# Optimization experiments

Measured on AMD Instinct MI355X. Metric: run time of the kernel, lower is better.

## Reference

```python
import jax, jax.numpy as jnp
import numpy as np

NUM_EXPERTS = 128
INPUT_DIM = 128
HIDDEN_DIM = 512
OUTPUT_DIM = 128
TOKENS_PER_EXPERT = 2048


def make_identity_experts(num_experts, input_dim, output_dim):
    # identical to the torch helper: zeros with ones on the (square) diagonal
    d = min(input_dim, output_dim)
    w = jnp.zeros((num_experts, input_dim, output_dim), dtype=jnp.float32)
    idx = jnp.arange(d)
    return w.at[:, idx, idx].set(1.0)


def setup_inputs() -> dict:
    key = jax.random.key(0)
    k_tok, = jax.random.split(key, 1)
    group_token = jax.random.normal(
        k_tok, (NUM_EXPERTS, TOKENS_PER_EXPERT, INPUT_DIM), dtype=jnp.float32)
    weights1 = make_identity_experts(NUM_EXPERTS, INPUT_DIM, HIDDEN_DIM)
    weights2 = make_identity_experts(NUM_EXPERTS, HIDDEN_DIM, OUTPUT_DIM)
    return {"group_token": group_token, "weights1": weights1, "weights2": weights2}


def reference(group_token, weights1, weights2):
    # grouped GEMM 1: per-expert [T, in] @ [in, hid]
    h = jnp.einsum('etd,edh->eth', group_token, weights1)
    # exact (erf-based) GELU, matching torch.nn.functional.gelu default
    h = jax.nn.gelu(h, approximate=False)
    # grouped GEMM 2: per-expert [T, hid] @ [hid, out]
    out = jnp.einsum('eth,eho->eto', h, weights2)
    return out
```

## Files before the change

kernel.cpp:

```cpp
#include <hip/hip_runtime.h>
#include <hip/hip_bf16.h>
#include <stdint.h>

typedef __attribute__((ext_vector_type(8))) short s8v;
typedef __attribute__((ext_vector_type(4))) short s4v;
typedef __attribute__((ext_vector_type(4))) float f4v;

#define NE   128
#define NT   2048
#define DIN  128
#define DH   512
#define DOUT 128

#define MFMA32(a,b,c) __builtin_amdgcn_mfma_f32_16x16x32_bf16(a,b,c,0,0,0)
#define MFMA16(a,b,c) __builtin_amdgcn_mfma_f32_16x16x16bf16_1k(a,b,c,0,0,0)

#define GLOAD16(g,l) __builtin_amdgcn_global_load_lds( \
    (const __attribute__((address_space(1))) void*)(g), \
    (__attribute__((address_space(3))) void*)(l), 16, 0, 0)

#define WAIT_VM(N) asm volatile("s_waitcnt vmcnt(" #N ")" ::: "memory")
#define BAR() do { asm volatile("" ::: "memory"); \
                   __builtin_amdgcn_s_barrier();  \
                   asm volatile("" ::: "memory"); } while (0)

__device__ __forceinline__ __hip_bfloat162 pk2(float a, float b) {
  float2 t; t.x = a; t.y = b;
  return __float22bfloat162_rn(t);
}

__device__ __forceinline__ s8v pack8(float4 a, float4 b) {
  union { s8v v; __hip_bfloat162 h[4]; } u;
  u.h[0] = pk2(a.x, a.y); u.h[1] = pk2(a.z, a.w);
  u.h[2] = pk2(b.x, b.y); u.h[3] = pk2(b.z, b.w);
  return u.v;
}

__device__ __forceinline__ float gelu_f(float x) {
  float x2 = x * x;
  float p  = __builtin_fmaf(x2, 0.07135481f, 1.5957691f);
  float e  = __expf(-x * p);
  return x * __builtin_amdgcn_rcpf(1.0f + e);
}

#define W1_BLOCKS (NE * 4)
__global__ __launch_bounds__(256) void pack_weights(
    const float* __restrict__ W1, const float* __restrict__ W2,
    ushort* __restrict__ W1F, ushort* __restrict__ W2F) {
  __shared__ __align__(16) float T[32 * 132];
  const int tid = threadIdx.x;

  if ((int)blockIdx.x < W1_BLOCKS) {
    const int e = blockIdx.x >> 2, ks = blockIdx.x & 3;
    const float* We = W1 + (size_t)e * (DIN * DH) + (size_t)(ks * 32) * DH;
    const int r = tid >> 3, c0 = (tid & 7) * 16;
    const int lane = tid & 63, wid = tid >> 6;
    const int q = lane >> 4, l16 = lane & 15;
    for (int hc = 0; hc < 4; ++hc) {
      if (hc) __syncthreads();
      const float* src = We + (size_t)r * DH + hc * 128 + c0;
      float4 v0 = *(const float4*)(src + 0);
      float4 v1 = *(const float4*)(src + 4);
      float4 v2 = *(const float4*)(src + 8);
      float4 v3 = *(const float4*)(src + 12);
      float* t = &T[r * 132 + c0];
      *(float4*)(t + 0) = v0; *(float4*)(t + 4)  = v1;
      *(float4*)(t + 8) = v2; *(float4*)(t + 12) = v3;
      __syncthreads();
#pragma unroll
      for (int i = 0; i < 2; ++i) {
        const int htl = wid + 4 * i;
        const int ht  = hc * 8 + htl;
        float g[8];
#pragma unroll
        for (int j = 0; j < 8; ++j) g[j] = T[(8 * q + j) * 132 + 16 * htl + l16];
        float4 a; a.x = g[0]; a.y = g[1]; a.z = g[2]; a.w = g[3];
        float4 b; b.x = g[4]; b.y = g[5]; b.z = g[6]; b.w = g[7];
        *(s8v*)(W1F + ((((size_t)e * 32 + ht) * 4) + ks) * 512 + lane * 8) = pack8(a, b);
      }
    }
  } else {
    const int bb = (int)blockIdx.x - W1_BLOCKS;
    const int e = bb >> 5, ht = bb & 31;
    float (*T2)[132] = (float (*)[132])T;
    const int h = tid >> 4, c16 = tid & 15;
    const float* src = W2 + (size_t)e * (DH * DOUT) + (size_t)(ht * 16 + h) * DOUT + c16 * 8;
    float4 v0 = *(const float4*)src;
    float4 v1 = *(const float4*)(src + 4);
    float* trow = &T2[h][c16 * 8];
    *(float4*)(trow + 0) = v0; *(float4*)(trow + 4) = v1;
    __syncthreads();
    const int lane = tid & 63;
    const int q = lane >> 4, l16 = lane & 15;
#pragma unroll
    for (int i = 0; i < 2; ++i) {
      int ot = (tid >> 6) + i * 4;
      float g0 = T2[4 * q + 0][ot * 16 + l16];
      float g1 = T2[4 * q + 1][ot * 16 + l16];
      float g2 = T2[4 * q + 2][ot * 16 + l16];
      float g3 = T2[4 * q + 3][ot * 16 + l16];
      union { s4v v; __hip_bfloat162 h2[2]; } u;
      u.h2[0] = pk2(g0, g1); u.h2[1] = pk2(g2, g3);
      *(s4v*)(W2F + (((size_t)e * 32 + ht) * 8 + ot) * 256 + lane * 4) = u.v;
    }
  }
}

__global__ __launch_bounds__(256, 4) void moe_fused(
    const float* __restrict__ X, const ushort* __restrict__ W1F,
    const ushort* __restrict__ W2F, float* __restrict__ Out) {
  __shared__ __align__(16) ushort W1s[2][4096];
  __shared__ __align__(16) ushort W2s[2][4096];

  const int tid  = threadIdx.x;
  const int lane = tid & 63;
  const int wid  = tid >> 6;
  const int q    = lane >> 4;
  const int l16  = lane & 15;

  const int bid  = blockIdx.x;
  const int wk   = ((bid & 7) << 8) | (bid >> 3);
  const int e    = wk >> 4;
  const int tile = wk & 15;

  const float* Xe  = X + ((size_t)e * NT + (size_t)tile * 128) * DIN;
  const ushort* W1e = W1F + (size_t)e * 65536;
  const ushort* W2e = W2F + (size_t)e * 65536;
  float* Oe = Out + ((size_t)e * NT + (size_t)tile * 128) * DOUT;

  s8v xf[2][4];
#pragma unroll
  for (int mt = 0; mt < 2; ++mt) {
#pragma unroll
    for (int ks = 0; ks < 4; ++ks) {
      const float* p = Xe + (size_t)(wid * 32 + mt * 16 + l16) * DIN + ks * 32 + q * 8;
      float4 v0 = *(const float4*)p;
      float4 v1 = *(const float4*)(p + 4);
      xf[mt][ks] = pack8(v0, v1);
    }
  }

  const f4v zero4 = {0.0f, 0.0f, 0.0f, 0.0f};
  f4v oacc[2][8];
#pragma unroll
  for (int mt = 0; mt < 2; ++mt)
#pragma unroll
    for (int ot = 0; ot < 8; ++ot) oacc[mt][ot] = zero4;

  auto stage = [&](int chunk, int b) {
    const ushort* g1 = W1e + chunk * 4096;
    const ushort* g2 = W2e + chunk * 4096;
#pragma unroll
    for (int i = 0; i < 2; ++i) {
      int u = i * 256 + tid;
      GLOAD16(g1 + u * 8, &W1s[b][u * 8]);
      GLOAD16(g2 + u * 8, &W2s[b][u * 8]);
    }
  };

  asm volatile("" ::: "memory");

  stage(0, 0);

  for (int c = 0; c < 16; ++c) {
    const int buf = c & 1;
    WAIT_VM(0);
    BAR();
    if (c < 15) stage(c + 1, buf ^ 1);

#pragma unroll
    for (int hl = 0; hl < 2; ++hl) {
      f4v hacc[2]; hacc[0] = zero4; hacc[1] = zero4;
#pragma unroll
      for (int kp = 0; kp < 2; ++kp) {
        s8v af0 = *(const s8v*)&W1s[buf][(hl * 4 + kp * 2 + 0) * 512 + lane * 8];
        s8v af1 = *(const s8v*)&W1s[buf][(hl * 4 + kp * 2 + 1) * 512 + lane * 8];
        __builtin_amdgcn_s_setprio(1);
        hacc[0] = MFMA32(af0, xf[0][kp * 2 + 0], hacc[0]);
        hacc[1] = MFMA32(af0, xf[1][kp * 2 + 0], hacc[1]);
        hacc[0] = MFMA32(af1, xf[0][kp * 2 + 1], hacc[0]);
        hacc[1] = MFMA32(af1, xf[1][kp * 2 + 1], hacc[1]);
        __builtin_amdgcn_s_setprio(0);
      }
      s4v a2[2];
#pragma unroll
      for (int mt = 0; mt < 2; ++mt) {
        union { s4v v; __hip_bfloat162 h2[2]; } u;
        u.h2[0] = pk2(gelu_f(hacc[mt][0]), gelu_f(hacc[mt][1]));
        u.h2[1] = pk2(gelu_f(hacc[mt][2]), gelu_f(hacc[mt][3]));
        a2[mt] = u.v;
      }
#pragma unroll
      for (int op = 0; op < 2; ++op) {
        s4v b0 = *(const s4v*)&W2s[buf][(hl * 8 + op * 4 + 0) * 256 + lane * 4];
        s4v b1 = *(const s4v*)&W2s[buf][(hl * 8 + op * 4 + 1) * 256 + lane * 4];
        s4v b2 = *(const s4v*)&W2s[buf][(hl * 8 + op * 4 + 2) * 256 + lane * 4];
        s4v b3 = *(const s4v*)&W2s[buf][(hl * 8 + op * 4 + 3) * 256 + lane * 4];
        __builtin_amdgcn_s_setprio(1);
        oacc[0][op * 4 + 0] = MFMA16(a2[0], b0, oacc[0][op * 4 + 0]);
        oacc[1][op * 4 + 0] = MFMA16(a2[1], b0, oacc[1][op * 4 + 0]);
        oacc[0][op * 4 + 1] = MFMA16(a2[0], b1, oacc[0][op * 4 + 1]);
        oacc[1][op * 4 + 1] = MFMA16(a2[1], b1, oacc[1][op * 4 + 1]);
        oacc[0][op * 4 + 2] = MFMA16(a2[0], b2, oacc[0][op * 4 + 2]);
        oacc[1][op * 4 + 2] = MFMA16(a2[1], b2, oacc[1][op * 4 + 2]);
        oacc[0][op * 4 + 3] = MFMA16(a2[0], b3, oacc[0][op * 4 + 3]);
        oacc[1][op * 4 + 3] = MFMA16(a2[1], b3, oacc[1][op * 4 + 3]);
        __builtin_amdgcn_s_setprio(0);
      }
    }
  }

#pragma unroll
  for (int mt = 0; mt < 2; ++mt) {
    const int mb = wid * 32 + mt * 16 + 4 * q;
#pragma unroll
    for (int ot = 0; ot < 8; ++ot) {
      float* p = Oe + (size_t)mb * DOUT + ot * 16 + l16;
      p[0 * DOUT] = oacc[mt][ot][0];
      p[1 * DOUT] = oacc[mt][ot][1];
      p[2 * DOUT] = oacc[mt][ot][2];
      p[3 * DOUT] = oacc[mt][ot][3];
    }
  }
}

extern "C" void kernel_launch(void* const* d_in, const int* in_sizes, int n_in,
                              void* d_out, int out_size, void* d_ws, size_t ws_size,
                              hipStream_t stream) {
  const float* X  = (const float*)d_in[0];
  const float* W1 = (const float*)d_in[1];
  const float* W2 = (const float*)d_in[2];
  float* Out = (float*)d_out;

  ushort* W1F = (ushort*)d_ws;
  ushort* W2F = (ushort*)d_ws + (size_t)NE * 65536;

  pack_weights<<<NE * 4 + NE * 32, 256, 0, stream>>>(W1, W2, W1F, W2F);
  moe_fused<<<NE * (NT / 128), 256, 0, stream>>>(X, W1F, W2F, Out);
}
```

Before: 336.7 us.

## Use K=32 bf16 MFMA for second GEMM by merging hidden sub-tiles

The second GEMM switches from 16x16x16 to 16x16x32 bf16 MFMA. Within each 32-wide hidden chunk, the two 16-wide GELU outputs are packed into one 8-element A fragment, halving the number of second-GEMM MFMA issues. The W2 pre-pack kernel is rewritten to emit the matching K=32 fragment layout, using half as many blocks with larger tiles. The cost is more live registers, since both hidden sub-tiles are held before the second GEMM runs.

```diff
diff --git a/kernel.cpp b/kernel.cpp
--- a/kernel.cpp
+++ b/kernel.cpp
@@ -3,7 +3,6 @@
 #include <stdint.h>
 
 typedef __attribute__((ext_vector_type(8))) short s8v;
-typedef __attribute__((ext_vector_type(4))) short s4v;
 typedef __attribute__((ext_vector_type(4))) float f4v;
 
 #define NE   128
@@ -13,7 +12,6 @@
 #define DOUT 128
 
 #define MFMA32(a,b,c) __builtin_amdgcn_mfma_f32_16x16x32_bf16(a,b,c,0,0,0)
-#define MFMA16(a,b,c) __builtin_amdgcn_mfma_f32_16x16x16bf16_1k(a,b,c,0,0,0)
 
 #define GLOAD16(g,l) __builtin_amdgcn_global_load_lds( \
     (const __attribute__((address_space(1))) void*)(g), \
@@ -43,19 +41,27 @@
   return x * __builtin_amdgcn_rcpf(1.0f + e);
 }
 
+__device__ __forceinline__ float4 gelu4(f4v v) {
+  float4 r;
+  r.x = gelu_f(v[0]); r.y = gelu_f(v[1]);
+  r.z = gelu_f(v[2]); r.w = gelu_f(v[3]);
+  return r;
+}
+
 #define W1_BLOCKS (NE * 4)
+#define W2_BLOCKS (NE * 16)
 __global__ __launch_bounds__(256) void pack_weights(
     const float* __restrict__ W1, const float* __restrict__ W2,
     ushort* __restrict__ W1F, ushort* __restrict__ W2F) {
   __shared__ __align__(16) float T[32 * 132];
   const int tid = threadIdx.x;
+  const int lane = tid & 63, wid = tid >> 6;
+  const int q = lane >> 4, l16 = lane & 15;
 
   if ((int)blockIdx.x < W1_BLOCKS) {
     const int e = blockIdx.x >> 2, ks = blockIdx.x & 3;
     const float* We = W1 + (size_t)e * (DIN * DH) + (size_t)(ks * 32) * DH;
     const int r = tid >> 3, c0 = (tid & 7) * 16;
-    const int lane = tid & 63, wid = tid >> 6;
-    const int q = lane >> 4, l16 = lane & 15;
     for (int hc = 0; hc < 4; ++hc) {
       if (hc) __syncthreads();
       const float* src = We + (size_t)r * DH + hc * 128 + c0;
@@ -81,27 +87,29 @@
     }
   } else {
     const int bb = (int)blockIdx.x - W1_BLOCKS;
-    const int e = bb >> 5, ht = bb & 31;
-    float (*T2)[132] = (float (*)[132])T;
-    const int h = tid >> 4, c16 = tid & 15;
-    const float* src = W2 + (size_t)e * (DH * DOUT) + (size_t)(ht * 16 + h) * DOUT + c16 * 8;
-    float4 v0 = *(const float4*)src;
+    const int e = bb >> 4, ct = bb & 15;
+    const int r = tid >> 3, c0 = (tid & 7) * 16;
+    const float* src = W2 + (size_t)e * (DH * DOUT) + (size_t)(ct * 32 + r) * DOUT + c0;
+    float4 v0 = *(const float4*)(src + 0);
     float4 v1 = *(const float4*)(src + 4);
-    float* trow = &T2[h][c16 * 8];
-    *(float4*)(trow + 0) = v0; *(float4*)(trow + 4) = v1;
+    float4 v2 = *(const float4*)(src + 8);
+    float4 v3 = *(const float4*)(src + 12);
+    float* t = &T[r * 132 + c0];
+    *(float4*)(t + 0) = v0; *(float4*)(t + 4)  = v1;
+    *(float4*)(t + 8) = v2; *(float4*)(t + 12) = v3;
     __syncthreads();
-    const int lane = tid & 63;
-    const int q = lane >> 4, l16 = lane & 15;
 #pragma unroll
     for (int i = 0; i < 2; ++i) {
-      int ot = (tid >> 6) + i * 4;
-      float g0 = T2[4 * q + 0][ot * 16 + l16];
-      float g1 = T2[4 * q + 1][ot * 16 + l16];
-      float g2 = T2[4 * q + 2][ot * 16 + l16];
-      float g3 = T2[4 * q + 3][ot * 16 + l16];
-      union { s4v v; __hip_bfloat162 h2[2]; } u;
-      u.h2[0] = pk2(g0, g1); u.h2[1] = pk2(g2, g3);
-      *(s4v*)(W2F + (((size_t)e * 32 + ht) * 8 + ot) * 256 + lane * 4) = u.v;
+      const int ot = wid + 4 * i;
+      float g[8];
+#pragma unroll
+      for (int j = 0; j < 8; ++j) {
+        const int sig = (j < 4) ? (4 * q + j) : (16 + 4 * q + (j - 4));
+        g[j] = T[sig * 132 + ot * 16 + l16];
+      }
+      float4 a; a.x = g[0]; a.y = g[1]; a.z = g[2]; a.w = g[3];
+      float4 b; b.x = g[4]; b.y = g[5]; b.z = g[6]; b.w = g[7];
+      *(s8v*)(W2F + (((size_t)e * 16 + ct) * 8 + ot) * 512 + lane * 8) = pack8(a, b);
     }
   }
 }
@@ -168,45 +176,47 @@
     BAR();
     if (c < 15) stage(c + 1, buf ^ 1);
 
-#pragma unroll
-    for (int hl = 0; hl < 2; ++hl) {
-      f4v hacc[2]; hacc[0] = zero4; hacc[1] = zero4;
-#pragma unroll
-      for (int kp = 0; kp < 2; ++kp) {
-        s8v af0 = *(const s8v*)&W1s[buf][(hl * 4 + kp * 2 + 0) * 512 + lane * 8];
-        s8v af1 = *(const s8v*)&W1s[buf][(hl * 4 + kp * 2 + 1) * 512 + lane * 8];
-        __builtin_amdgcn_s_setprio(1);
-        hacc[0] = MFMA32(af0, xf[0][kp * 2 + 0], hacc[0]);
-        hacc[1] = MFMA32(af0, xf[1][kp * 2 + 0], hacc[1]);
-        hacc[0] = MFMA32(af1, xf[0][kp * 2 + 1], hacc[0]);
-        hacc[1] = MFMA32(af1, xf[1][kp * 2 + 1], hacc[1]);
-        __builtin_amdgcn_s_setprio(0);
-      }
-      s4v a2[2];
-#pragma unroll
-      for (int mt = 0; mt < 2; ++mt) {
-        union { s4v v; __hip_bfloat162 h2[2]; } u;
-        u.h2[0] = pk2(gelu_f(hacc[mt][0]), gelu_f(hacc[mt][1]));
-        u.h2[1] = pk2(gelu_f(hacc[mt][2]), gelu_f(hacc[mt][3]));
-        a2[mt] = u.v;
-      }
-#pragma unroll
-      for (int op = 0; op < 2; ++op) {
-        s4v b0 = *(const s4v*)&W2s[buf][(hl * 8 + op * 4 + 0) * 256 + lane * 4];
-        s4v b1 = *(const s4v*)&W2s[buf][(hl * 8 + op * 4 + 1) * 256 + lane * 4];
-        s4v b2 = *(const s4v*)&W2s[buf][(hl * 8 + op * 4 + 2) * 256 + lane * 4];
-        s4v b3 = *(const s4v*)&W2s[buf][(hl * 8 + op * 4 + 3) * 256 + lane * 4];
-        __builtin_amdgcn_s_setprio(1);
-        oacc[0][op * 4 + 0] = MFMA16(a2[0], b0, oacc[0][op * 4 + 0]);
-        oacc[1][op * 4 + 0] = MFMA16(a2[1], b0, oacc[1][op * 4 + 0]);
-        oacc[0][op * 4 + 1] = MFMA16(a2[0], b1, oacc[0][op * 4 + 1]);
-        oacc[1][op * 4 + 1] = MFMA16(a2[1], b1, oacc[1][op * 4 + 1]);
-        oacc[0][op * 4 + 2] = MFMA16(a2[0], b2, oacc[0][op * 4 + 2]);
-        oacc[1][op * 4 + 2] = MFMA16(a2[1], b2, oacc[1][op * 4 + 2]);
-        oacc[0][op * 4 + 3] = MFMA16(a2[0], b3, oacc[0][op * 4 + 3]);
-        oacc[1][op * 4 + 3] = MFMA16(a2[1], b3, oacc[1][op * 4 + 3]);
-        __builtin_amdgcn_s_setprio(0);
-      }
+    f4v h0[2]; h0[0] = zero4; h0[1] = zero4;
+#pragma unroll
+    for (int kp = 0; kp < 2; ++kp) {
+      s8v af0 = *(const s8v*)&W1s[buf][(kp * 2 + 0) * 512 + lane * 8];
+      s8v af1 = *(const s8v*)&W1s[buf][(kp * 2 + 1) * 512 + lane * 8];
+      __builtin_amdgcn_s_setprio(1);
+      h0[0] = MFMA32(af0, xf[0][kp * 2 + 0], h0[0]);
+      h0[1] = MFMA32(af0, xf[1][kp * 2 + 0], h0[1]);
+      h0[0] = MFMA32(af1, xf[0][kp * 2 + 1], h0[0]);
+      h0[1] = MFMA32(af1, xf[1][kp * 2 + 1], h0[1]);
+      __builtin_amdgcn_s_setprio(0);
+    }
+    float4 ga0 = gelu4(h0[0]);
+    float4 ga1 = gelu4(h0[1]);
+
+    f4v h1[2]; h1[0] = zero4; h1[1] = zero4;
+#pragma unroll
+    for (int kp = 0; kp < 2; ++kp) {
+      s8v af0 = *(const s8v*)&W1s[buf][(4 + kp * 2 + 0) * 512 + lane * 8];
+      s8v af1 = *(const s8v*)&W1s[buf][(4 + kp * 2 + 1) * 512 + lane * 8];
+      __builtin_amdgcn_s_setprio(1);
+      h1[0] = MFMA32(af0, xf[0][kp * 2 + 0], h1[0]);
+      h1[1] = MFMA32(af0, xf[1][kp * 2 + 0], h1[1]);
+      h1[0] = MFMA32(af1, xf[0][kp * 2 + 1], h1[0]);
+      h1[1] = MFMA32(af1, xf[1][kp * 2 + 1], h1[1]);
+      __builtin_amdgcn_s_setprio(0);
+    }
+
+    s8v a8_0 = pack8(ga0, gelu4(h1[0]));
+    s8v a8_1 = pack8(ga1, gelu4(h1[1]));
+
+#pragma unroll
+    for (int op = 0; op < 4; ++op) {
+      s8v b0 = *(const s8v*)&W2s[buf][(op * 2 + 0) * 512 + lane * 8];
+      s8v b1 = *(const s8v*)&W2s[buf][(op * 2 + 1) * 512 + lane * 8];
+      __builtin_amdgcn_s_setprio(1);
+      oacc[0][op * 2 + 0] = MFMA32(a8_0, b0, oacc[0][op * 2 + 0]);
+      oacc[1][op * 2 + 0] = MFMA32(a8_1, b0, oacc[1][op * 2 + 0]);
+      oacc[0][op * 2 + 1] = MFMA32(a8_0, b1, oacc[0][op * 2 + 1]);
+      oacc[1][op * 2 + 1] = MFMA32(a8_1, b1, oacc[1][op * 2 + 1]);
+      __builtin_amdgcn_s_setprio(0);
     }
   }
 
@@ -235,6 +245,6 @@
   ushort* W1F = (ushort*)d_ws;
   ushort* W2F = (ushort*)d_ws + (size_t)NE * 65536;
 
-  pack_weights<<<NE * 4 + NE * 32, 256, 0, stream>>>(W1, W2, W1F, W2F);
+  pack_weights<<<W1_BLOCKS + W2_BLOCKS, 256, 0, stream>>>(W1, W2, W1F, W2F);
   moe_fused<<<NE * (NT / 128), 256, 0, stream>>>(X, W1F, W2F, Out);
 }
```

New measurement: 371.3 us. 1.1x slower.
